# Optimization experiments

Hardware: AMD Instinct MI355X
Metric: run time of the kernel (lower is better)

Reference implementation:

```python
import jax, jax.numpy as jnp
import numpy as np


def _gru_cell(x, h, Wih, Whh, bih, bhh):
    # torch nn.GRU cell math: gates ordered [r, z, n]
    gi = Wih @ x + bih
    gh = Whh @ h + bhh
    ir, iz, inn = jnp.split(gi, 3)
    hr, hz, hn = jnp.split(gh, 3)
    r = jax.nn.sigmoid(ir + hr)
    z = jax.nn.sigmoid(iz + hz)
    n = jnp.tanh(inn + r * hn)
    return (1.0 - z) * n + z * h


def _lrelu(x):
    # torch nn.LeakyReLU default negative_slope=0.01
    return jnp.where(x >= 0, x, 0.01 * x)


def setup_inputs() -> dict:
    key = jax.random.key(0)
    ks = jax.random.split(key, 24)
    V, E, H, C, S, T = 32000, 512, 1024, 2048, 256, 129
    w = lambda k, shape: jax.random.normal(k, shape, jnp.float32) * 0.02
    return {
        "inputs": jax.random.randint(ks[0], (T,), 0, V),
        "h1": jax.random.normal(ks[1], (H,), jnp.float32),
        "h2": jax.random.normal(ks[2], (H,), jnp.float32),
        "projected_keys": jax.random.normal(ks[3], (S, H), jnp.float32),
        "encoder_outputs": jax.random.normal(ks[4], (S, C), jnp.float32),
        "embeds": jax.random.normal(ks[5], (V, E), jnp.float32),
        "Wq": w(ks[6], (H, H)),
        "v_att": w(ks[7], (H,)),
        "W_ih1": w(ks[8], (3 * H, E + C)),
        "W_hh1": w(ks[9], (3 * H, H)),
        "b_ih1": w(ks[10], (3 * H,)),
        "b_hh1": w(ks[11], (3 * H,)),
        "W_ih2": w(ks[12], (3 * H, H + C)),
        "W_hh2": w(ks[13], (3 * H, H)),
        "b_ih2": w(ks[14], (3 * H,)),
        "b_hh2": w(ks[15], (3 * H,)),
        "W_pre": w(ks[16], (H, E + H + C)),
        "b_pre": w(ks[17], (H,)),
        "W_out": w(ks[18], (E, H)),
        "b_out": w(ks[19], (E,)),
    }


def reference(inputs, h1, h2, projected_keys, encoder_outputs, embeds, Wq, v_att,
              W_ih1, W_hh1, b_ih1, b_hh1, W_ih2, W_hh2, b_ih2, b_hh2,
              W_pre, b_pre, W_out, b_out):
    # teacher_forcing = 1.0 -> decoder input at step i is inputs[i] (ground truth)
    emb_seq = embeds[inputs[:-1]]  # [T-1, E]

    def step(carry, emb):
        h1, h2 = carry
        # additive attention: query from top-layer hidden state
        q = Wq @ h2                                     # [H]
        e = jnp.tanh(projected_keys + q) @ v_att        # [S]
        alphas = jax.nn.softmax(e)                      # [S]
        context = alphas @ encoder_outputs              # [C]
        h1n = _gru_cell(jnp.concatenate([emb, context]), h1, W_ih1, W_hh1, b_ih1, b_hh1)
        o1 = _lrelu(h1n)                                # dropout identity (eval)
        h2n = _gru_cell(jnp.concatenate([o1, context]), h2, W_ih2, W_hh2, b_ih2, b_hh2)
        o2 = _lrelu(h2n)
        pre = _lrelu(W_pre @ jnp.concatenate([emb, o2, context]) + b_pre)  # [H]
        out = W_out @ o2 + b_out                        # [E]
        return (h1n, h2n), (out, pre, alphas)

    (h1f, h2f), (outs, pres, alphas) = jax.lax.scan(step, (h1, h2), emb_seq)
    # torch.cat(outputs, dim=1) of [1,1,E] pieces -> [1, T-1, E]
    return outs[None], pres[None], alphas, h1f, h2f
```

## Files before the change

kernel.cpp:

```cpp
#include <hip/hip_runtime.h>

typedef unsigned int uint32;
typedef unsigned long long u64;

#define GBLK 256
#define BT 512
#define NSTEP 128

#define QE    0
#define EE    1024
#define CTXE  1280
#define H1E   3328
#define H2E   4352
#define O1E   5376
#define O2E   6400
#define GH1E  7424
#define GH2E  10496

struct Params {
  const int* inputs;
  const float *h1_in, *h2_in, *embeds, *vatt;
  const float *pk, *enc, *Wq, *Wih1, *Whh1, *Wih2, *Whh2, *Wpre, *Wout;
  const float *bih1, *bhh1, *bih2, *bhh2, *bpre, *bout;
  float* out;
  float* ws;
};

__device__ __forceinline__ float blo(uint32 u) { return __uint_as_float(u << 16); }
__device__ __forceinline__ float bhi(uint32 u) { return __uint_as_float(u & 0xffff0000u); }
__device__ __forceinline__ uint32 bfr(float f) {
  uint32 u = __float_as_uint(f);
  return (u + 0x7fffu + ((u >> 16) & 1u)) >> 16;
}

__device__ __forceinline__ u64 ald64(const u64* a) {
  return __hip_atomic_load(a, __ATOMIC_RELAXED, __HIP_MEMORY_SCOPE_AGENT);
}
__device__ __forceinline__ void ast64(u64* a, u64 v) {
  __hip_atomic_store(a, v, __ATOMIC_RELAXED, __HIP_MEMORY_SCOPE_AGENT);
}
__device__ __forceinline__ u64 pk64(float f, uint32 ep) {
  return ((u64)ep << 32) | (u64)__float_as_uint(f);
}
__device__ __forceinline__ float lo32f(u64 v) { return __uint_as_float((uint32)v); }
__device__ __forceinline__ bool tok(u64 v, uint32 tg) { return (uint32)(v >> 32) >= tg; }

__device__ __forceinline__ float wsum(float v) {
#pragma unroll
  for (int o = 32; o; o >>= 1) v += __shfl_xor(v, o, 64);
  return v;
}

__device__ __forceinline__ void ldchunk(const float* W, size_t base, int lane, uint32* r) {
  const float* wf = W + base + lane * 8;
  float4 a = *(const float4*)wf;
  float4 c = *(const float4*)(wf + 4);
  r[0] = bfr(a.x) | (bfr(a.y) << 16);
  r[1] = bfr(a.z) | (bfr(a.w) << 16);
  r[2] = bfr(c.x) | (bfr(c.y) << 16);
  r[3] = bfr(c.z) | (bfr(c.w) << 16);
}

__device__ __forceinline__ float dotchunk(const uint32* r, const float* xc, int lane) {
  const float* x = xc + lane * 8;
  float4 x0 = *(const float4*)x, x1 = *(const float4*)(x + 4);
  return blo(r[0]) * x0.x + bhi(r[0]) * x0.y + blo(r[1]) * x0.z + bhi(r[1]) * x0.w +
         blo(r[2]) * x1.x + bhi(r[2]) * x1.y + blo(r[3]) * x1.z + bhi(r[3]) * x1.w;
}

__device__ __forceinline__ float sigm(float x) { return 1.f / (1.f + expf(-x)); }
__device__ __forceinline__ float lrelu(float x) { return x >= 0.f ? x : 0.01f * x; }

__global__ __launch_bounds__(BT, 2) void dec_flow_kernel(Params p) {
  __shared__ float sx[8192];
  __shared__ float s_red[8];
  __shared__ float s_part[72];

  const int tid = threadIdx.x;
  const int lane = tid & 63;
  const int w = tid >> 6;
  const int b = blockIdx.x;
  const int gw = b * 8 + w;
  const int i0 = b * 4;
  const int j0 = b * 8;

  u64* wsu = (u64*)p.ws;

  float* outs = p.out;
  float* pres = p.out + 65536;
  float* alph = p.out + 196608;
  float* h1f = p.out + 229376;
  float* h2f = p.out + 230400;

  uint32 wa[48];
  if (gw < 1024) {
#pragma unroll
    for (int c = 0; c < 7; ++c)
      ldchunk(p.Wpre, (size_t)gw * 3584 + c * 512, lane, wa + 4 * c);
    ldchunk(p.Whh1, (size_t)gw * 1024, lane, wa + 28);
    ldchunk(p.Whh1, (size_t)gw * 1024 + 512, lane, wa + 32);
    ldchunk(p.Whh1, (size_t)(gw + 1024) * 1024, lane, wa + 36);
    ldchunk(p.Whh1, (size_t)(gw + 1024) * 1024 + 512, lane, wa + 40);
    wa[44] = wa[45] = wa[46] = wa[47] = 0u;
  } else {
    const int widx = gw - 1024;
    ldchunk(p.Whh1, (size_t)(2048 + widx) * 1024, lane, wa + 0);
    ldchunk(p.Whh1, (size_t)(2048 + widx) * 1024 + 512, lane, wa + 4);
#pragma unroll
    for (int r = 0; r < 3; ++r) {
      ldchunk(p.Whh2, (size_t)(widx + r * 1024) * 1024, lane, wa + 8 + 8 * r);
      ldchunk(p.Whh2, (size_t)(widx + r * 1024) * 1024 + 512, lane, wa + 12 + 8 * r);
    }
    ldchunk(p.Wq, (size_t)widx * 1024, lane, wa + 32);
    ldchunk(p.Wq, (size_t)widx * 1024 + 512, lane, wa + 36);
    const int wr = widx & 511;
    ldchunk(p.Wout, (size_t)wr * 1024, lane, wa + 40);
    ldchunk(p.Wout, (size_t)wr * 1024 + 512, lane, wa + 44);
  }

  uint32 wd[32];
#pragma unroll
  for (int k = 0; k < 8; ++k) {
    const int mm = w + 8 * k;
    const int mmc = mm < 60 ? mm : 0;
    const int r = mmc / 15, m = mmc % 15, g = m / 5, c = m % 5;
    ldchunk(p.Wih1, (size_t)(g * 1024 + i0 + r) * 2560 + c * 512, lane, wd + 4 * k);
  }

  uint32 we9[36];
#pragma unroll
  for (int k = 0; k < 9; ++k) {
    const int mm = w + 8 * k;
    const int r = mm / 18, m = mm % 18, g = m / 6, c = m % 6;
    ldchunk(p.Wih2, (size_t)(g * 1024 + i0 + r) * 3072 + c * 512, lane, we9 + 4 * k);
  }

  uint32 wenc[4] = {0u, 0u, 0u, 0u};
  if (tid < 256) {
    const float* er = p.enc + (size_t)tid * 2048 + j0;
    float4 a = *(const float4*)er, c = *(const float4*)(er + 4);
    wenc[0] = bfr(a.x) | (bfr(a.y) << 16);
    wenc[1] = bfr(a.z) | (bfr(a.w) << 16);
    wenc[2] = bfr(c.x) | (bfr(c.y) << 16);
    wenc[3] = bfr(c.z) | (bfr(c.w) << 16);
  }

  const int d0 = tid * 2;
  const float pk0 = p.pk[(size_t)b * 1024 + d0];
  const float pk1 = p.pk[(size_t)b * 1024 + d0 + 1];
  const float va0 = p.vatt[d0];
  const float va1 = p.vatt[d0 + 1];

  if (gw < 16) ast64(wsu + H1E + gw * 64 + lane, pk64(p.h1_in[gw * 64 + lane], 1));
  else if (gw < 32) ast64(wsu + H2E + (gw - 16) * 64 + lane, pk64(p.h2_in[(gw - 16) * 64 + lane], 1));

  for (int t = 0; t <= NSTEP; ++t) {
    const uint32 TP = (uint32)(t + 1);
    const uint32 TS = (uint32)(t + 2);

    if (t < NSTEP) {
      {
        const u64 *a0 = wsu + H1E + tid, *a1 = wsu + H1E + 512 + tid;
        const u64 *a2 = wsu + H2E + tid, *a3 = wsu + H2E + 512 + tid;
        u64 v0, v1, v2, v3;
        for (;;) {
          v0 = ald64(a0); v1 = ald64(a1); v2 = ald64(a2); v3 = ald64(a3);
          if (tok(v0, TP) && tok(v1, TP) && tok(v2, TP) && tok(v3, TP)) break;
          __builtin_amdgcn_s_sleep(1);
        }
        sx[6144 + tid] = lo32f(v0); sx[6656 + tid] = lo32f(v1);
        sx[7168 + tid] = lo32f(v2); sx[7680 + tid] = lo32f(v3);
      }
      __syncthreads();
      if (gw >= 1024) {
        const int widx = gw - 1024;
        float sq = dotchunk(wa + 32, sx + 7168, lane) + dotchunk(wa + 36, sx + 7680, lane);
        sq = wsum(sq);
        if (lane == 0) ast64(wsu + QE + widx, pk64(sq, TS));
        float s = dotchunk(wa + 0, sx + 6144, lane) + dotchunk(wa + 4, sx + 6656, lane);
        s = wsum(s);
        if (lane == 0) ast64(wsu + GH1E + 2048 + widx, pk64(s + p.bhh1[2048 + widx], TS));
#pragma unroll
        for (int r = 0; r < 3; ++r) {
          float t2 = dotchunk(wa + 8 + 8 * r, sx + 7168, lane) +
                     dotchunk(wa + 12 + 8 * r, sx + 7680, lane);
          t2 = wsum(t2);
          if (lane == 0) ast64(wsu + GH2E + widx + 1024 * r, pk64(t2 + p.bhh2[widx + 1024 * r], TS));
        }
      } else {
        float s1 = dotchunk(wa + 28, sx + 6144, lane) + dotchunk(wa + 32, sx + 6656, lane);
        s1 = wsum(s1);
        if (lane == 0) ast64(wsu + GH1E + gw, pk64(s1 + p.bhh1[gw], TS));
        float s2 = dotchunk(wa + 36, sx + 6144, lane) + dotchunk(wa + 40, sx + 6656, lane);
        s2 = wsum(s2);
        if (lane == 0) ast64(wsu + GH1E + 1024 + gw, pk64(s2 + p.bhh1[1024 + gw], TS));
      }
    }

    if (t > 0) {
      {
        const float* embp = p.embeds + (size_t)p.inputs[t - 1] * 512;
        float ev = embp[tid];
        const u64 *a0 = wsu + O2E + tid, *a1 = wsu + O2E + 512 + tid;
        const u64 *c0 = wsu + CTXE + tid, *c1 = wsu + CTXE + 512 + tid;
        const u64 *c2 = wsu + CTXE + 1024 + tid, *c3 = wsu + CTXE + 1536 + tid;
        u64 v0, v1, u0, u1, u2, u3;
        for (;;) {
          v0 = ald64(a0); v1 = ald64(a1);
          u0 = ald64(c0); u1 = ald64(c1); u2 = ald64(c2); u3 = ald64(c3);
          if (tok(v0, TP) && tok(v1, TP) && tok(u0, TP) && tok(u1, TP) &&
              tok(u2, TP) && tok(u3, TP)) break;
          __builtin_amdgcn_s_sleep(1);
        }
        sx[tid] = ev;
        sx[512 + tid] = lo32f(v0); sx[1024 + tid] = lo32f(v1);
        sx[1536 + tid] = lo32f(u0); sx[2048 + tid] = lo32f(u1);
        sx[2560 + tid] = lo32f(u2); sx[3072 + tid] = lo32f(u3);
      }
      __syncthreads();
      if (gw < 1024) {
        float s = 0.f;
#pragma unroll
        for (int c = 0; c < 7; ++c) s += dotchunk(wa + 4 * c, sx + 512 * c, lane);
        s = wsum(s);
        if (lane == 0) pres[(size_t)(t - 1) * 1024 + gw] = lrelu(s + p.bpre[gw]);
      } else if (gw - 1024 < 512) {
        const int widx = gw - 1024;
        float so = dotchunk(wa + 40, sx + 512, lane) + dotchunk(wa + 44, sx + 1024, lane);
        so = wsum(so);
        if (lane == 0) outs[(size_t)(t - 1) * 512 + widx] = so + p.bout[widx];
      }
    }
    if (t == NSTEP) break;

    {
      float q0, q1;
      {
        const u64 *a0 = wsu + QE + d0, *a1 = wsu + QE + d0 + 1;
        u64 v0, v1;
        for (;;) {
          v0 = ald64(a0); v1 = ald64(a1);
          if (tok(v0, TS) && tok(v1, TS)) break;
          __builtin_amdgcn_s_sleep(1);
        }
        q0 = lo32f(v0); q1 = lo32f(v1);
      }
      float acc = va0 * tanhf(pk0 + q0) + va1 * tanhf(pk1 + q1);
      acc = wsum(acc);
      if (lane == 0) s_red[w] = acc;
      __syncthreads();
      if (tid == 0) {
        float e = s_red[0] + s_red[1] + s_red[2] + s_red[3] +
                  s_red[4] + s_red[5] + s_red[6] + s_red[7];
        ast64(wsu + EE + b, pk64(e, TS));
      }
      __syncthreads();
      float e_i = 0.f, pe = 0.f;
      if (tid < 256) {
        u64 v = ald64(wsu + EE + tid);
        while (!tok(v, TS)) { __builtin_amdgcn_s_sleep(1); v = ald64(wsu + EE + tid); }
        e_i = lo32f(v);
        float mw = e_i;
#pragma unroll
        for (int o = 32; o; o >>= 1) mw = fmaxf(mw, __shfl_xor(mw, o, 64));
        if (lane == 0) s_red[w] = mw;
      }
      __syncthreads();
      float m = fmaxf(fmaxf(s_red[0], s_red[1]), fmaxf(s_red[2], s_red[3]));
      __syncthreads();
      if (tid < 256) {
        pe = expf(e_i - m);
        float zw = wsum(pe);
        if (lane == 0) s_red[w] = zw;
      }
      __syncthreads();
      float Z = s_red[0] + s_red[1] + s_red[2] + s_red[3];
      if (tid < 256) {
        float alpha = pe / Z;
        if (b == 0) alph[(size_t)t * 256 + tid] = alpha;
        float c[8];
        c[0] = alpha * blo(wenc[0]); c[1] = alpha * bhi(wenc[0]);
        c[2] = alpha * blo(wenc[1]); c[3] = alpha * bhi(wenc[1]);
        c[4] = alpha * blo(wenc[2]); c[5] = alpha * bhi(wenc[2]);
        c[6] = alpha * blo(wenc[3]); c[7] = alpha * bhi(wenc[3]);
#pragma unroll
        for (int o = 32; o; o >>= 1) {
#pragma unroll
          for (int j = 0; j < 8; ++j) c[j] += __shfl_xor(c[j], o, 64);
        }
        if (lane == 0) {
#pragma unroll
          for (int j = 0; j < 8; ++j) s_part[w * 8 + j] = c[j];
        }
      }
      __syncthreads();
      if (tid < 8) {
        float cj = s_part[tid] + s_part[8 + tid] + s_part[16 + tid] + s_part[24 + tid];
        ast64(wsu + CTXE + j0 + tid, pk64(cj, TS));
      }
    }

    {
      float g1a = 0.f, g1b = 0.f, g1c = 0.f, h1old = 0.f;
      if (tid < 4) {
        const int i = i0 + tid;
        u64 x0, x1, x2;
        for (;;) {
          x0 = ald64(wsu + GH1E + i); x1 = ald64(wsu + GH1E + 1024 + i);
          x2 = ald64(wsu + GH1E + 2048 + i);
          if (tok(x0, TS) && tok(x1, TS) && tok(x2, TS)) break;
          __builtin_amdgcn_s_sleep(1);
        }
        g1a = lo32f(x0); g1b = lo32f(x1); g1c = lo32f(x2);
        h1old = sx[6144 + i];
      }
      {
        const float* embc = p.embeds + (size_t)p.inputs[t] * 512;
        float ev = embc[tid];
        const u64 *c0 = wsu + CTXE + tid, *c1 = wsu + CTXE + 512 + tid;
        const u64 *c2 = wsu + CTXE + 1024 + tid, *c3 = wsu + CTXE + 1536 + tid;
        u64 u0, u1, u2, u3;
        for (;;) {
          u0 = ald64(c0); u1 = ald64(c1); u2 = ald64(c2); u3 = ald64(c3);
          if (tok(u0, TS) && tok(u1, TS) && tok(u2, TS) && tok(u3, TS)) break;
          __builtin_amdgcn_s_sleep(1);
        }
        sx[tid] = ev;
        sx[512 + tid] = lo32f(u0); sx[1024 + tid] = lo32f(u1);
        sx[1536 + tid] = lo32f(u2); sx[2048 + tid] = lo32f(u3);
      }
      __syncthreads();
#pragma unroll
      for (int k = 0; k < 8; ++k) {
        const int mm = w + 8 * k;
        if (mm < 60) {
          const int c = (mm % 15) % 5;
          float s = dotchunk(wd + 4 * k, sx + c * 512, lane);
          s = wsum(s);
          if (lane == 0) s_part[mm] = s;
        }
      }
      __syncthreads();
      if (tid < 4) {
        const int i = i0 + tid;
        const float* sp = s_part + tid * 15;
        float sr = sp[0] + sp[1] + sp[2] + sp[3] + sp[4];
        float sz = sp[5] + sp[6] + sp[7] + sp[8] + sp[9];
        float sn = sp[10] + sp[11] + sp[12] + sp[13] + sp[14];
        float r = sigm(sr + p.bih1[i] + g1a);
        float z = sigm(sz + p.bih1[1024 + i] + g1b);
        float n = tanhf(sn + p.bih1[2048 + i] + r * g1c);
        float h = (1.f - z) * n + z * h1old;
        ast64(wsu + H1E + i, pk64(h, TS));
        ast64(wsu + O1E + i, pk64(lrelu(h), TS));
      }
    }

    {
      float g2a = 0.f, g2b = 0.f, g2c = 0.f, h2old = 0.f;
      if (tid < 4) {
        const int i = i0 + tid;
        u64 x0, x1, x2;
        for (;;) {
          x0 = ald64(wsu + GH2E + i); x1 = ald64(wsu + GH2E + 1024 + i);
          x2 = ald64(wsu + GH2E + 2048 + i);
          if (tok(x0, TS) && tok(x1, TS) && tok(x2, TS)) break;
          __builtin_amdgcn_s_sleep(1);
        }
        g2a = lo32f(x0); g2b = lo32f(x1); g2c = lo32f(x2);
        h2old = sx[7168 + i];
      }
      {
        const u64 *a0 = wsu + O1E + tid, *a1 = wsu + O1E + 512 + tid;
        u64 v0, v1;
        for (;;) {
          v0 = ald64(a0); v1 = ald64(a1);
          if (tok(v0, TS) && tok(v1, TS)) break;
          __builtin_amdgcn_s_sleep(1);
        }
        sx[2560 + tid] = lo32f(v0); sx[3072 + tid] = lo32f(v1);
      }
      __syncthreads();
#pragma unroll
      for (int k = 0; k < 9; ++k) {
        const int mm = w + 8 * k;
        const int c = (mm % 18) % 6;
        const float* xp = (c < 2) ? (sx + 2560 + c * 512) : (sx + 512 + (c - 2) * 512);
        float s = dotchunk(we9 + 4 * k, xp, lane);
        s = wsum(s);
        if (lane == 0) s_part[mm] = s;
      }
      __syncthreads();
      if (tid < 4) {
        const int i = i0 + tid;
        const float* sp = s_part + tid * 18;
        float sr = sp[0] + sp[1] + sp[2] + sp[3] + sp[4] + sp[5];
        float sz = sp[6] + sp[7] + sp[8] + sp[9] + sp[10] + sp[11];
        float sn = sp[12] + sp[13] + sp[14] + sp[15] + sp[16] + sp[17];
        float r = sigm(sr + p.bih2[i] + g2a);
        float z = sigm(sz + p.bih2[1024 + i] + g2b);
        float n = tanhf(sn + p.bih2[2048 + i] + r * g2c);
        float h = (1.f - z) * n + z * h2old;
        ast64(wsu + H2E + i, pk64(h, TS));
        ast64(wsu + O2E + i, pk64(lrelu(h), TS));
      }
    }
  }

  if (gw < 16) {
    u64 v = ald64(wsu + H1E + gw * 64 + lane);
    while (!tok(v, NSTEP + 1)) { __builtin_amdgcn_s_sleep(1); v = ald64(wsu + H1E + gw * 64 + lane); }
    h1f[gw * 64 + lane] = lo32f(v);
  } else if (gw < 32) {
    u64 v = ald64(wsu + H2E + (gw - 16) * 64 + lane);
    while (!tok(v, NSTEP + 1)) { __builtin_amdgcn_s_sleep(1); v = ald64(wsu + H2E + (gw - 16) * 64 + lane); }
    h2f[(gw - 16) * 64 + lane] = lo32f(v);
  }
}

extern "C" void kernel_launch(void* const* d_in, const int* in_sizes, int n_in,
                              void* d_out, int out_size, void* d_ws, size_t ws_size,
                              hipStream_t stream) {
  hipMemsetAsync(d_ws, 0, 131072, stream);

  Params p;
  p.inputs = (const int*)d_in[0];
  p.h1_in = (const float*)d_in[1];
  p.h2_in = (const float*)d_in[2];
  p.pk = (const float*)d_in[3];
  p.enc = (const float*)d_in[4];
  p.embeds = (const float*)d_in[5];
  p.Wq = (const float*)d_in[6];
  p.vatt = (const float*)d_in[7];
  p.Wih1 = (const float*)d_in[8];
  p.Whh1 = (const float*)d_in[9];
  p.bih1 = (const float*)d_in[10];
  p.bhh1 = (const float*)d_in[11];
  p.Wih2 = (const float*)d_in[12];
  p.Whh2 = (const float*)d_in[13];
  p.bih2 = (const float*)d_in[14];
  p.bhh2 = (const float*)d_in[15];
  p.Wpre = (const float*)d_in[16];
  p.bpre = (const float*)d_in[17];
  p.Wout = (const float*)d_in[18];
  p.bout = (const float*)d_in[19];
  p.out = (float*)d_out;
  p.ws = (float*)d_ws;

  void* args[] = {&p};
  hipError_t err = hipLaunchCooperativeKernel((const void*)dec_flow_kernel,
                                              dim3(GBLK), dim3(BT), args, 0, stream);
  if (err != hipSuccess) {
    dec_flow_kernel<<<dim3(GBLK), dim3(BT), 0, stream>>>(p);
  }
}
```

Baseline: 6.434 ms.

## Replace per-element epoch-tagged flags with sharded arrival counters

Inter-block dataflow signalling changes from 64-bit value+epoch words polled per element to plain float values plus per-stage arrival counters sharded across 8 cache lines. One thread polls each counter and then the whole block bulk-loads the data with cache-bypassing dwordx4 loads. The attention score reduction moves earlier, right after q is produced, and the gate outputs are packed as float4 per row. This cuts the bytes and atomics each poll touches. In exchange every stage now needs explicit vmcnt drains and block barriers before a counter is incremented, and correctness depends on that ordering holding across blocks.

```diff
diff --git a/kernel.cpp b/kernel.cpp
--- a/kernel.cpp
+++ b/kernel.cpp
@@ -1,21 +1,26 @@
 #include <hip/hip_runtime.h>
 
 typedef unsigned int uint32;
-typedef unsigned long long u64;
 
 #define GBLK 256
 #define BT 512
 #define NSTEP 128
 
-#define QE    0
-#define EE    1024
-#define CTXE  1280
-#define H1E   3328
-#define H2E   4352
-#define O1E   5376
-#define O2E   6400
-#define GH1E  7424
-#define GH2E  10496
+#define CQ   0
+#define CGH  1
+#define CE   2
+#define CCTX 3
+#define CH1  4
+#define CH2  5
+#define QF    1024
+#define EF    2048
+#define CTXF  2304
+#define H1FO  4352
+#define H2FO  5376
+#define O1F   6400
+#define O2F   7424
+#define GH1F  8448
+#define GH2F  12544
 
 struct Params {
   const int* inputs;
@@ -33,17 +38,38 @@
   return (u + 0x7fffu + ((u >> 16) & 1u)) >> 16;
 }
 
-__device__ __forceinline__ u64 ald64(const u64* a) {
+__device__ __forceinline__ float ald(const float* a) {
   return __hip_atomic_load(a, __ATOMIC_RELAXED, __HIP_MEMORY_SCOPE_AGENT);
 }
-__device__ __forceinline__ void ast64(u64* a, u64 v) {
+__device__ __forceinline__ void ast(float* a, float v) {
   __hip_atomic_store(a, v, __ATOMIC_RELAXED, __HIP_MEMORY_SCOPE_AGENT);
 }
-__device__ __forceinline__ u64 pk64(float f, uint32 ep) {
-  return ((u64)ep << 32) | (u64)__float_as_uint(f);
-}
-__device__ __forceinline__ float lo32f(u64 v) { return __uint_as_float((uint32)v); }
-__device__ __forceinline__ bool tok(u64 v, uint32 tg) { return (uint32)(v >> 32) >= tg; }
+
+__device__ __forceinline__ float4 cld16(const float* p) {
+  float4 r;
+  asm volatile("global_load_dwordx4 %0, %1, off sc0 sc1\n\ts_waitcnt vmcnt(0)"
+               : "=&v"(r) : "v"(p) : "memory");
+  return r;
+}
+
+#define VDRAIN() asm volatile("s_waitcnt vmcnt(0)" ::: "memory")
+
+__device__ __forceinline__ void cadd(int* wsi, int c, int b) {
+  __hip_atomic_fetch_add(wsi + c * 128 + (b & 7) * 16, 1,
+                         __ATOMIC_RELAXED, __HIP_MEMORY_SCOPE_AGENT);
+}
+__device__ __forceinline__ void cpoll(const int* wsi, int c, int tgt) {
+  const int* base = wsi + c * 128;
+  for (;;) {
+    bool ok = true;
+#pragma unroll
+    for (int k = 0; k < 8; ++k)
+      ok &= (__hip_atomic_load(base + k * 16, __ATOMIC_RELAXED,
+                               __HIP_MEMORY_SCOPE_AGENT) >= tgt);
+    if (ok) return;
+    __builtin_amdgcn_s_sleep(1);
+  }
+}
 
 __device__ __forceinline__ float wsum(float v) {
 #pragma unroll
@@ -71,7 +97,7 @@
 __device__ __forceinline__ float sigm(float x) { return 1.f / (1.f + expf(-x)); }
 __device__ __forceinline__ float lrelu(float x) { return x >= 0.f ? x : 0.01f * x; }
 
-__global__ __launch_bounds__(BT, 2) void dec_flow_kernel(Params p) {
+__global__ __launch_bounds__(BT, 2) void dec_cnt_kernel(Params p) {
   __shared__ float sx[8192];
   __shared__ float s_red[8];
   __shared__ float s_part[72];
@@ -84,7 +110,7 @@
   const int i0 = b * 4;
   const int j0 = b * 8;
 
-  u64* wsu = (u64*)p.ws;
+  int* wsi = (int*)p.ws;
 
   float* outs = p.out;
   float* pres = p.out + 65536;
@@ -136,6 +162,7 @@
   }
 
   uint32 wenc[4] = {0u, 0u, 0u, 0u};
+  float4 pk4 = {0.f, 0.f, 0.f, 0.f}, va4 = {0.f, 0.f, 0.f, 0.f};
   if (tid < 256) {
     const float* er = p.enc + (size_t)tid * 2048 + j0;
     float4 a = *(const float4*)er, c = *(const float4*)(er + 4);
@@ -143,90 +170,103 @@
     wenc[1] = bfr(a.z) | (bfr(a.w) << 16);
     wenc[2] = bfr(c.x) | (bfr(c.y) << 16);
     wenc[3] = bfr(c.z) | (bfr(c.w) << 16);
-  }
-
-  const int d0 = tid * 2;
-  const float pk0 = p.pk[(size_t)b * 1024 + d0];
-  const float pk1 = p.pk[(size_t)b * 1024 + d0 + 1];
-  const float va0 = p.vatt[d0];
-  const float va1 = p.vatt[d0 + 1];
-
-  if (gw < 16) ast64(wsu + H1E + gw * 64 + lane, pk64(p.h1_in[gw * 64 + lane], 1));
-  else if (gw < 32) ast64(wsu + H2E + (gw - 16) * 64 + lane, pk64(p.h2_in[(gw - 16) * 64 + lane], 1));
+    pk4 = *(const float4*)(p.pk + (size_t)b * 1024 + 4 * tid);
+    va4 = *(const float4*)(p.vatt + 4 * tid);
+  }
+
+  if (tid < 4) {
+    ast(p.ws + H1FO + i0 + tid, p.h1_in[i0 + tid]);
+    ast(p.ws + H2FO + i0 + tid, p.h2_in[i0 + tid]);
+  }
+  VDRAIN();
+  if (tid == 0) { cadd(wsi, CH1, b); cadd(wsi, CH2, b); }
 
   for (int t = 0; t <= NSTEP; ++t) {
-    const uint32 TP = (uint32)(t + 1);
-    const uint32 TS = (uint32)(t + 2);
-
     if (t < NSTEP) {
-      {
-        const u64 *a0 = wsu + H1E + tid, *a1 = wsu + H1E + 512 + tid;
-        const u64 *a2 = wsu + H2E + tid, *a3 = wsu + H2E + 512 + tid;
-        u64 v0, v1, v2, v3;
-        for (;;) {
-          v0 = ald64(a0); v1 = ald64(a1); v2 = ald64(a2); v3 = ald64(a3);
-          if (tok(v0, TP) && tok(v1, TP) && tok(v2, TP) && tok(v3, TP)) break;
-          __builtin_amdgcn_s_sleep(1);
-        }
-        sx[6144 + tid] = lo32f(v0); sx[6656 + tid] = lo32f(v1);
-        sx[7168 + tid] = lo32f(v2); sx[7680 + tid] = lo32f(v3);
-      }
-      __syncthreads();
-      if (gw >= 1024) {
+      if (tid == 0) { cpoll(wsi, CH1, 32 * (t + 1)); cpoll(wsi, CH2, 32 * (t + 1)); }
+      __syncthreads();
+      if (tid < 256 || b >= 128) {
+        const float* hsrc = (tid < 256) ? (p.ws + H1FO + 4 * tid)
+                                        : (p.ws + H2FO + 4 * (tid - 256));
+        float4 hv = cld16(hsrc);
+        *(float4*)&sx[6144 + 4 * tid] = hv;
+      }
+      __syncthreads();
+      if (b >= 128) {
         const int widx = gw - 1024;
         float sq = dotchunk(wa + 32, sx + 7168, lane) + dotchunk(wa + 36, sx + 7680, lane);
         sq = wsum(sq);
-        if (lane == 0) ast64(wsu + QE + widx, pk64(sq, TS));
+        if (lane == 0) ast(p.ws + QF + widx, sq);
+        VDRAIN();
+        __syncthreads();
+        if (tid == 0) cadd(wsi, CQ, b);
         float s = dotchunk(wa + 0, sx + 6144, lane) + dotchunk(wa + 4, sx + 6656, lane);
         s = wsum(s);
-        if (lane == 0) ast64(wsu + GH1E + 2048 + widx, pk64(s + p.bhh1[2048 + widx], TS));
+        if (lane == 0) ast(p.ws + GH1F + widx * 4 + 2, s + p.bhh1[2048 + widx]);
 #pragma unroll
         for (int r = 0; r < 3; ++r) {
           float t2 = dotchunk(wa + 8 + 8 * r, sx + 7168, lane) +
                      dotchunk(wa + 12 + 8 * r, sx + 7680, lane);
           t2 = wsum(t2);
-          if (lane == 0) ast64(wsu + GH2E + widx + 1024 * r, pk64(t2 + p.bhh2[widx + 1024 * r], TS));
+          if (lane == 0) ast(p.ws + GH2F + widx * 4 + r, t2 + p.bhh2[widx + 1024 * r]);
         }
+        VDRAIN();
+        __syncthreads();
+        if (tid == 0) cadd(wsi, CGH, b);
       } else {
         float s1 = dotchunk(wa + 28, sx + 6144, lane) + dotchunk(wa + 32, sx + 6656, lane);
         s1 = wsum(s1);
-        if (lane == 0) ast64(wsu + GH1E + gw, pk64(s1 + p.bhh1[gw], TS));
+        if (lane == 0) ast(p.ws + GH1F + gw * 4 + 0, s1 + p.bhh1[gw]);
         float s2 = dotchunk(wa + 36, sx + 6144, lane) + dotchunk(wa + 40, sx + 6656, lane);
         s2 = wsum(s2);
-        if (lane == 0) ast64(wsu + GH1E + 1024 + gw, pk64(s2 + p.bhh1[1024 + gw], TS));
+        if (lane == 0) ast(p.ws + GH1F + gw * 4 + 1, s2 + p.bhh1[1024 + gw]);
+        VDRAIN();
+        __syncthreads();
+        if (tid == 0) cadd(wsi, CGH, b);
+      }
+
+      if (tid == 0) cpoll(wsi, CQ, 16 * (t + 1));
+      __syncthreads();
+      if (tid < 256) {
+        float4 qv = cld16(p.ws + QF + 4 * tid);
+        float acc = va4.x * tanhf(pk4.x + qv.x) + va4.y * tanhf(pk4.y + qv.y) +
+                    va4.z * tanhf(pk4.z + qv.z) + va4.w * tanhf(pk4.w + qv.w);
+        acc = wsum(acc);
+        if (lane == 0) s_red[w] = acc;
+      }
+      __syncthreads();
+      if (tid == 0) {
+        float e = s_red[0] + s_red[1] + s_red[2] + s_red[3];
+        ast(p.ws + EF + b, e);
+        VDRAIN();
+        cadd(wsi, CE, b);
       }
     }
 
     if (t > 0) {
-      {
-        const float* embp = p.embeds + (size_t)p.inputs[t - 1] * 512;
-        float ev = embp[tid];
-        const u64 *a0 = wsu + O2E + tid, *a1 = wsu + O2E + 512 + tid;
-        const u64 *c0 = wsu + CTXE + tid, *c1 = wsu + CTXE + 512 + tid;
-        const u64 *c2 = wsu + CTXE + 1024 + tid, *c3 = wsu + CTXE + 1536 + tid;
-        u64 v0, v1, u0, u1, u2, u3;
-        for (;;) {
-          v0 = ald64(a0); v1 = ald64(a1);
-          u0 = ald64(c0); u1 = ald64(c1); u2 = ald64(c2); u3 = ald64(c3);
-          if (tok(v0, TP) && tok(v1, TP) && tok(u0, TP) && tok(u1, TP) &&
-              tok(u2, TP) && tok(u3, TP)) break;
-          __builtin_amdgcn_s_sleep(1);
-        }
-        sx[tid] = ev;
-        sx[512 + tid] = lo32f(v0); sx[1024 + tid] = lo32f(v1);
-        sx[1536 + tid] = lo32f(u0); sx[2048 + tid] = lo32f(u1);
-        sx[2560 + tid] = lo32f(u2); sx[3072 + tid] = lo32f(u3);
+      if (t == NSTEP) {
+        if (tid == 0) cpoll(wsi, CH2, 32 * (t + 1));
+      }
+      __syncthreads();
+      if (tid < 256) {
+        float4 v = cld16(p.ws + O2F + 4 * tid);
+        *(float4*)&sx[2560 + 4 * tid] = v;
       }
       __syncthreads();
       if (gw < 1024) {
         float s = 0.f;
 #pragma unroll
-        for (int c = 0; c < 7; ++c) s += dotchunk(wa + 4 * c, sx + 512 * c, lane);
+        for (int c = 0; c < 7; ++c) {
+          const float* xp = (c == 0) ? sx
+                          : (c <= 2) ? (sx + 2560 + (c - 1) * 512)
+                                     : (sx + 512 + (c - 3) * 512);
+          s += dotchunk(wa + 4 * c, xp, lane);
+        }
         s = wsum(s);
         if (lane == 0) pres[(size_t)(t - 1) * 1024 + gw] = lrelu(s + p.bpre[gw]);
       } else if (gw - 1024 < 512) {
         const int widx = gw - 1024;
-        float so = dotchunk(wa + 40, sx + 512, lane) + dotchunk(wa + 44, sx + 1024, lane);
+        float so = dotchunk(wa + 40, sx + 2560, lane) + dotchunk(wa + 44, sx + 3072, lane);
         so = wsum(so);
         if (lane == 0) outs[(size_t)(t - 1) * 512 + widx] = so + p.bout[widx];
       }
@@ -234,32 +274,16 @@
     if (t == NSTEP) break;
 
     {
-      float q0, q1;
-      {
-        const u64 *a0 = wsu + QE + d0, *a1 = wsu + QE + d0 + 1;
-        u64 v0, v1;
-        for (;;) {
-          v0 = ald64(a0); v1 = ald64(a1);
-          if (tok(v0, TS) && tok(v1, TS)) break;
-          __builtin_amdgcn_s_sleep(1);
-        }
-        q0 = lo32f(v0); q1 = lo32f(v1);
-      }
-      float acc = va0 * tanhf(pk0 + q0) + va1 * tanhf(pk1 + q1);
-      acc = wsum(acc);
-      if (lane == 0) s_red[w] = acc;
-      __syncthreads();
-      if (tid == 0) {
-        float e = s_red[0] + s_red[1] + s_red[2] + s_red[3] +
-                  s_red[4] + s_red[5] + s_red[6] + s_red[7];
-        ast64(wsu + EE + b, pk64(e, TS));
+      if (tid == 0) cpoll(wsi, CE, 32 * (t + 1));
+      __syncthreads();
+      if (tid < 64) {
+        float4 ev = cld16(p.ws + EF + 4 * tid);
+        *(float4*)&sx[4096 + 4 * tid] = ev;
       }
       __syncthreads();
       float e_i = 0.f, pe = 0.f;
       if (tid < 256) {
-        u64 v = ald64(wsu + EE + tid);
-        while (!tok(v, TS)) { __builtin_amdgcn_s_sleep(1); v = ald64(wsu + EE + tid); }
-        e_i = lo32f(v);
+        e_i = sx[4096 + tid];
         float mw = e_i;
 #pragma unroll
         for (int o = 32; o; o >>= 1) mw = fmaxf(mw, __shfl_xor(mw, o, 64));
@@ -296,38 +320,26 @@
       __syncthreads();
       if (tid < 8) {
         float cj = s_part[tid] + s_part[8 + tid] + s_part[16 + tid] + s_part[24 + tid];
-        ast64(wsu + CTXE + j0 + tid, pk64(cj, TS));
-      }
+        ast(p.ws + CTXF + j0 + tid, cj);
+      }
+      VDRAIN();
+      if (tid == 0) cadd(wsi, CCTX, b);
     }
 
     {
-      float g1a = 0.f, g1b = 0.f, g1c = 0.f, h1old = 0.f;
+      if (tid == 0) { cpoll(wsi, CCTX, 32 * (t + 1)); cpoll(wsi, CGH, 32 * (t + 1)); }
+      __syncthreads();
+      const float* embc = p.embeds + (size_t)p.inputs[t] * 512;
+      sx[tid] = embc[tid];
+      {
+        float4 cv = cld16(p.ws + CTXF + 4 * tid);
+        *(float4*)&sx[512 + 4 * tid] = cv;
+      }
+      float4 g1 = {0.f, 0.f, 0.f, 0.f};
+      float h1old = 0.f;
       if (tid < 4) {
-        const int i = i0 + tid;
-        u64 x0, x1, x2;
-        for (;;) {
-          x0 = ald64(wsu + GH1E + i); x1 = ald64(wsu + GH1E + 1024 + i);
-          x2 = ald64(wsu + GH1E + 2048 + i);
-          if (tok(x0, TS) && tok(x1, TS) && tok(x2, TS)) break;
-          __builtin_amdgcn_s_sleep(1);
-        }
-        g1a = lo32f(x0); g1b = lo32f(x1); g1c = lo32f(x2);
-        h1old = sx[6144 + i];
-      }
-      {
-        const float* embc = p.embeds + (size_t)p.inputs[t] * 512;
-        float ev = embc[tid];
-        const u64 *c0 = wsu + CTXE + tid, *c1 = wsu + CTXE + 512 + tid;
-        const u64 *c2 = wsu + CTXE + 1024 + tid, *c3 = wsu + CTXE + 1536 + tid;
-        u64 u0, u1, u2, u3;
-        for (;;) {
-          u0 = ald64(c0); u1 = ald64(c1); u2 = ald64(c2); u3 = ald64(c3);
-          if (tok(u0, TS) && tok(u1, TS) && tok(u2, TS) && tok(u3, TS)) break;
-          __builtin_amdgcn_s_sleep(1);
-        }
-        sx[tid] = ev;
-        sx[512 + tid] = lo32f(u0); sx[1024 + tid] = lo32f(u1);
-        sx[1536 + tid] = lo32f(u2); sx[2048 + tid] = lo32f(u3);
+        g1 = cld16(p.ws + GH1F + (i0 + tid) * 4);
+        h1old = ald(p.ws + H1FO + i0 + tid);
       }
       __syncthreads();
 #pragma unroll
@@ -347,38 +359,29 @@
         float sr = sp[0] + sp[1] + sp[2] + sp[3] + sp[4];
         float sz = sp[5] + sp[6] + sp[7] + sp[8] + sp[9];
         float sn = sp[10] + sp[11] + sp[12] + sp[13] + sp[14];
-        float r = sigm(sr + p.bih1[i] + g1a);
-        float z = sigm(sz + p.bih1[1024 + i] + g1b);
-        float n = tanhf(sn + p.bih1[2048 + i] + r * g1c);
+        float r = sigm(sr + p.bih1[i] + g1.x);
+        float z = sigm(sz + p.bih1[1024 + i] + g1.y);
+        float n = tanhf(sn + p.bih1[2048 + i] + r * g1.z);
         float h = (1.f - z) * n + z * h1old;
-        ast64(wsu + H1E + i, pk64(h, TS));
-        ast64(wsu + O1E + i, pk64(lrelu(h), TS));
-      }
+        ast(p.ws + H1FO + i, h);
+        ast(p.ws + O1F + i, lrelu(h));
+      }
+      VDRAIN();
+      if (tid == 0) cadd(wsi, CH1, b);
     }
 
     {
-      float g2a = 0.f, g2b = 0.f, g2c = 0.f, h2old = 0.f;
+      if (tid == 0) cpoll(wsi, CH1, 32 * (t + 2));
+      __syncthreads();
+      if (tid < 256) {
+        float4 ov = cld16(p.ws + O1F + 4 * tid);
+        *(float4*)&sx[2560 + 4 * tid] = ov;
+      }
+      float4 g2 = {0.f, 0.f, 0.f, 0.f};
+      float h2old = 0.f;
       if (tid < 4) {
-        const int i = i0 + tid;
-        u64 x0, x1, x2;
-        for (;;) {
-          x0 = ald64(wsu + GH2E + i); x1 = ald64(wsu + GH2E + 1024 + i);
-          x2 = ald64(wsu + GH2E + 2048 + i);
-          if (tok(x0, TS) && tok(x1, TS) && tok(x2, TS)) break;
-          __builtin_amdgcn_s_sleep(1);
-        }
-        g2a = lo32f(x0); g2b = lo32f(x1); g2c = lo32f(x2);
-        h2old = sx[7168 + i];
-      }
-      {
-        const u64 *a0 = wsu + O1E + tid, *a1 = wsu + O1E + 512 + tid;
-        u64 v0, v1;
-        for (;;) {
-          v0 = ald64(a0); v1 = ald64(a1);
-          if (tok(v0, TS) && tok(v1, TS)) break;
-          __builtin_amdgcn_s_sleep(1);
-        }
-        sx[2560 + tid] = lo32f(v0); sx[3072 + tid] = lo32f(v1);
+        g2 = cld16(p.ws + GH2F + (i0 + tid) * 4);
+        h2old = ald(p.ws + H2FO + i0 + tid);
       }
       __syncthreads();
 #pragma unroll
@@ -397,31 +400,28 @@
         float sr = sp[0] + sp[1] + sp[2] + sp[3] + sp[4] + sp[5];
         float sz = sp[6] + sp[7] + sp[8] + sp[9] + sp[10] + sp[11];
         float sn = sp[12] + sp[13] + sp[14] + sp[15] + sp[16] + sp[17];
-        float r = sigm(sr + p.bih2[i] + g2a);
-        float z = sigm(sz + p.bih2[1024 + i] + g2b);
-        float n = tanhf(sn + p.bih2[2048 + i] + r * g2c);
+        float r = sigm(sr + p.bih2[i] + g2.x);
+        float z = sigm(sz + p.bih2[1024 + i] + g2.y);
+        float n = tanhf(sn + p.bih2[2048 + i] + r * g2.z);
         float h = (1.f - z) * n + z * h2old;
-        ast64(wsu + H2E + i, pk64(h, TS));
-        ast64(wsu + O2E + i, pk64(lrelu(h), TS));
-      }
-    }
-  }
-
-  if (gw < 16) {
-    u64 v = ald64(wsu + H1E + gw * 64 + lane);
-    while (!tok(v, NSTEP + 1)) { __builtin_amdgcn_s_sleep(1); v = ald64(wsu + H1E + gw * 64 + lane); }
-    h1f[gw * 64 + lane] = lo32f(v);
-  } else if (gw < 32) {
-    u64 v = ald64(wsu + H2E + (gw - 16) * 64 + lane);
-    while (!tok(v, NSTEP + 1)) { __builtin_amdgcn_s_sleep(1); v = ald64(wsu + H2E + (gw - 16) * 64 + lane); }
-    h2f[(gw - 16) * 64 + lane] = lo32f(v);
+        ast(p.ws + H2FO + i, h);
+        ast(p.ws + O2F + i, lrelu(h));
+      }
+      VDRAIN();
+      if (tid == 0) cadd(wsi, CH2, b);
+    }
+  }
+
+  if (tid < 4) {
+    h1f[i0 + tid] = ald(p.ws + H1FO + i0 + tid);
+    h2f[i0 + tid] = ald(p.ws + H2FO + i0 + tid);
   }
 }
 
 extern "C" void kernel_launch(void* const* d_in, const int* in_sizes, int n_in,
                               void* d_out, int out_size, void* d_ws, size_t ws_size,
                               hipStream_t stream) {
-  hipMemsetAsync(d_ws, 0, 131072, stream);
+  (void)hipMemsetAsync(d_ws, 0, 4096, stream);
 
   Params p;
   p.inputs = (const int*)d_in[0];
@@ -448,9 +448,9 @@
   p.ws = (float*)d_ws;
 
   void* args[] = {&p};
-  hipError_t err = hipLaunchCooperativeKernel((const void*)dec_flow_kernel,
+  hipError_t err = hipLaunchCooperativeKernel((const void*)dec_cnt_kernel,
                                               dim3(GBLK), dim3(BT), args, 0, stream);
   if (err != hipSuccess) {
-    dec_flow_kernel<<<dim3(GBLK), dim3(BT), 0, stream>>>(p);
-  }
-}
+    dec_cnt_kernel<<<dim3(GBLK), dim3(BT), 0, stream>>>(p);
+  }
+}
```

Measured after the change: 6.061 ms. 5.8% less time.
